# Performance work log

Hardware: AMD Instinct MI355X
Metric: run time of the kernel (lower is better)

Reference implementation:

```python
import jax, jax.numpy as jnp
import numpy as np

DIM = 256      # C
TOPK = 32      # topk_win_num
WIN = 8        # winSize
G = 64         # g (shift group size); 4*G == DIM here


def setup_inputs() -> dict:
    key = jax.random.key(0)
    k0, k1, k2, k3 = jax.random.split(key, 4)
    B, Nt, Ns, C = 32, 256, 4096, DIM
    z = jax.random.normal(k0, (B, Nt, C), jnp.float32)
    x = jax.random.normal(k1, (B, Ns, C), jnp.float32)
    # shift_op_down: Conv2d(C, 4g, 1) -> weight [4g, C]; shift_op_up: Conv2d(4g, C, 1)
    Wd = jax.random.normal(k2, (4 * G, C), jnp.float32) * 0.05
    bd = jnp.zeros((4 * G,), jnp.float32)
    Wu = jax.random.normal(k3, (C, 4 * G), jnp.float32) * 0.05
    bu = jnp.zeros((C,), jnp.float32)
    return {"z": z, "x": x, "Wd": Wd, "bd": bd, "Wu": Wu, "bu": bu}


def reference(z, x, Wd, bd, Wu, bu):
    B, Nt, C = z.shape
    Ns = x.shape[1]
    hs = int(np.sqrt(Ns))
    wn = hs // WIN          # windows per side
    wsa = WIN * WIN         # tokens per window
    K = TOPK

    # AdaptiveMaxPool2d((1,1)) over template tokens -> global max per channel
    z_max = jnp.max(z, axis=1)                               # [B, C]
    sim = jnp.einsum('bc,bnc->bn', z_max, x) / C             # [B, Ns]
    # per-window mean similarity
    sim = sim.reshape(B, wn, WIN, wn, WIN).transpose(0, 1, 3, 2, 4)
    sim = sim.reshape(B, wn * wn, wsa).mean(-1)              # [B, wn*wn]
    idx = jax.lax.top_k(sim, K)[1]                           # [B, K]

    # windowed view of search tokens: [B, wn*wn, wsa, C]
    x_win = x.reshape(B, wn, WIN, wn, WIN, C).transpose(0, 1, 3, 2, 4, 5)
    x_win = x_win.reshape(B, wn * wn, wsa, C)
    x_sel = jnp.take_along_axis(x_win, idx[:, :, None, None], axis=1)  # [B, K, wsa, C]

    xe = x_sel.reshape(B * K, WIN, WIN, C)                   # NHWC per selected window
    t = xe @ Wd.T + bd                                       # 1x1 conv down -> [n, h, w, 4G]

    # 4-direction spatial shift by 1 (zero fill), one channel group per direction
    g0, g1, g2, g3 = t[..., :G], t[..., G:2 * G], t[..., 2 * G:3 * G], t[..., 3 * G:]
    s0 = jnp.pad(g0[:, :, 1:, :], ((0, 0), (0, 0), (0, 1), (0, 0)))  # shift left  (W)
    s1 = jnp.pad(g1[:, :, :-1, :], ((0, 0), (0, 0), (1, 0), (0, 0)))  # shift right (W)
    s2 = jnp.pad(g2[:, 1:, :, :], ((0, 0), (0, 1), (0, 0), (0, 0)))  # shift up    (H)
    s3 = jnp.pad(g3[:, :-1, :, :], ((0, 0), (1, 0), (0, 0), (0, 0)))  # shift down  (H)
    sh = jnp.concatenate([s0, s1, s2, s3], axis=-1)          # [n, h, w, 4G]

    up = sh @ Wu.T + bu                                      # 1x1 conv up -> [n, h, w, C]
    out = (xe + up).reshape(B, K * WIN * WIN, C)             # [B, K*wsa, C]
    return out
```

## Files before the change

kernel.cpp:

```cpp
#include <hip/hip_runtime.h>
#include <hip/hip_bf16.h>

#define C_DIM 256
#define B_SZ 32
#define NS 4096
#define NT_Z 256
#define TOPK_K 32
#define NWIN 64
#define WTOK 64

typedef __attribute__((ext_vector_type(8))) short short8;
typedef __attribute__((ext_vector_type(4))) float f32x4;

static __device__ inline unsigned short f2b(float f) {
  union { float f; unsigned int u; } x; x.f = f;
  unsigned int u = x.u;
  return (unsigned short)((u + 0x7FFFu + ((u >> 16) & 1u)) >> 16);
}
static __device__ inline float b2f(unsigned int h16) {
  union { unsigned int u; float f; } x; x.u = h16 << 16;
  return x.f;
}

__global__ void prep_kernel(const float* __restrict__ Wd, const float* __restrict__ Wu,
                            unsigned short* __restrict__ Wdb, unsigned short* __restrict__ Wub,
                            const float* __restrict__ z, float* __restrict__ zpart) {
  int blk = blockIdx.x;
  if (blk < 64) {
    int i = blk * 256 + threadIdx.x;
    float4 a = ((const float4*)Wd)[i];
    float4 c = ((const float4*)Wu)[i];
    ushort4 ha, hc;
    ha.x = f2b(a.x); ha.y = f2b(a.y); ha.z = f2b(a.z); ha.w = f2b(a.w);
    hc.x = f2b(c.x); hc.y = f2b(c.y); hc.z = f2b(c.z); hc.w = f2b(c.w);
    ((ushort4*)Wdb)[i] = ha;
    ((ushort4*)Wub)[i] = hc;
  } else {
    int i = blk - 64;
    int b = i >> 3, ch = i & 7;
    int c = threadIdx.x;
    const float* p = z + ((size_t)b * NT_Z + ch * 32) * C_DIM + c;
    float m = p[0];
    for (int n = 1; n < 32; ++n) m = fmaxf(m, p[(size_t)n * C_DIM]);
    zpart[(size_t)i * C_DIM + c] = m;
  }
}

__global__ __launch_bounds__(256) void winscore_kernel(const float* __restrict__ x,
                                                       const float* __restrict__ zpart,
                                                       float* __restrict__ score) {
  int b = blockIdx.x >> 6;
  int w = blockIdx.x & 63;
  int wy = w >> 3, wx = w & 7;

  __shared__ float zs[C_DIM];
  {
    float m = zpart[(size_t)(b * 8) * C_DIM + threadIdx.x];
    #pragma unroll
    for (int ch = 1; ch < 8; ++ch)
      m = fmaxf(m, zpart[(size_t)(b * 8 + ch) * C_DIM + threadIdx.x]);
    zs[threadIdx.x] = m;
  }
  __syncthreads();

  int wv = threadIdx.x >> 6;
  int ln = threadIdx.x & 63;

  float a0 = 0.f, a1 = 0.f, a2 = 0.f, a3 = 0.f;
  for (int t = 0; t < 16; ++t) {
    int tok = wv * 16 + t;
    int iy = tok >> 3, ix = tok & 7;
    int n = (wy * 8 + iy) * 64 + wx * 8 + ix;
    const float4 v = *(const float4*)(x + ((size_t)b * NS + n) * C_DIM + ln * 4);
    a0 += v.x; a1 += v.y; a2 += v.z; a3 += v.w;
  }
  const float4 z4 = ((const float4*)zs)[ln];
  float p = a0 * z4.x + a1 * z4.y + a2 * z4.z + a3 * z4.w;
  for (int off = 32; off >= 1; off >>= 1) p += __shfl_xor(p, off);

  __shared__ float wsum[4];
  if (ln == 0) wsum[wv] = p;
  __syncthreads();
  if (threadIdx.x == 0) score[blockIdx.x] = wsum[0] + wsum[1] + wsum[2] + wsum[3];
}

__global__ __launch_bounds__(512, 4) void fused_win(
    const float* __restrict__ x, const float* __restrict__ score,
    const unsigned short* __restrict__ Wdb, const unsigned short* __restrict__ Wub,
    const float* __restrict__ bd, const float* __restrict__ bu,
    float* __restrict__ out)
{
  __shared__ unsigned short xe_s[WTOK * C_DIM];
  __shared__ unsigned short t_s[WTOK * C_DIM];
  __shared__ float sc[NWIN];
  __shared__ int wsel_s;

  const int bk = blockIdx.x;
  const int b = bk >> 5;
  const int kk = bk & 31;
  const int tid = threadIdx.x;

  if (tid < NWIN) sc[tid] = score[b * NWIN + tid];
  __syncthreads();
  if (tid < NWIN) {
    float v = sc[tid];
    int rank = 0;
    #pragma unroll
    for (int j = 0; j < NWIN; ++j) {
      float sj = sc[j];
      rank += (sj > v) || (sj == v && j < tid);
    }
    if (rank == kk) wsel_s = tid;
  }
  __syncthreads();
  const int wsel = wsel_s;
  const int wy = wsel >> 3, wx = wsel & 7;

  const int wv = tid >> 6;
  const int ln = tid & 63;
  const int lr = ln & 15;
  const int lg = ln >> 4;

  const unsigned short* wdbase = Wdb + ((size_t)(wv * 32 + lr)) * C_DIM + lg * 8;
  const unsigned short* wubase = Wub + ((size_t)(wv * 32 + lr)) * C_DIM + lg * 8;

  short8 wreg[8][2];
  #pragma unroll
  for (int ks = 0; ks < 8; ++ks)
    #pragma unroll
    for (int nt = 0; nt < 2; ++nt)
      wreg[ks][nt] = *(const short8*)(wdbase + nt * 16 * C_DIM + ks * 32);

  {
    const int c4 = tid & 63;
    const int m0 = tid >> 6;
    const float* xb = x + (size_t)b * NS * C_DIM + c4 * 4;
    float4 xv[8];
    #pragma unroll
    for (int i = 0; i < 8; ++i) {
      int m = m0 + i * 8;
      int n = (wy * 8 + (m >> 3)) * 64 + wx * 8 + (m & 7);
      xv[i] = *(const float4*)(xb + (size_t)n * C_DIM);
    }
    #pragma unroll
    for (int i = 0; i < 8; ++i) {
      int m = m0 + i * 8;
      ushort4 h;
      h.x = f2b(xv[i].x); h.y = f2b(xv[i].y); h.z = f2b(xv[i].z); h.w = f2b(xv[i].w);
      int byteoff = m * 512 + ((c4 * 8) ^ ((m & 7) << 4));
      *(ushort4*)((char*)xe_s + byteoff) = h;
    }
  }
  __syncthreads();

  f32x4 acc[4][2];
  #pragma unroll
  for (int a = 0; a < 4; ++a)
    #pragma unroll
    for (int n2 = 0; n2 < 2; ++n2) acc[a][n2] = (f32x4){0.f, 0.f, 0.f, 0.f};

  #pragma unroll
  for (int ks = 0; ks < 8; ++ks) {
    const int kb = ks * 64 + lg * 16;
    short8 af[4];
    #pragma unroll
    for (int mt = 0; mt < 4; ++mt) {
      int m = mt * 16 + lr;
      af[mt] = *(const short8*)((const char*)xe_s + m * 512 + (kb ^ ((m & 7) << 4)));
    }
    #pragma unroll
    for (int mt = 0; mt < 4; ++mt)
      #pragma unroll
      for (int nt = 0; nt < 2; ++nt)
        acc[mt][nt] = __builtin_amdgcn_mfma_f32_16x16x32_bf16(af[mt], wreg[ks][nt], acc[mt][nt], 0, 0, 0);
  }

  #pragma unroll
  for (int nt = 0; nt < 2; ++nt) {
    int o = wv * 32 + nt * 16 + lr;
    float bdv = bd[o];
    #pragma unroll
    for (int mt = 0; mt < 4; ++mt) {
      #pragma unroll
      for (int r = 0; r < 4; ++r) {
        int m = mt * 16 + lg * 4 + r;
        float v = acc[mt][nt][r] + bdv;
        *(unsigned short*)((char*)t_s + m * 512 + ((o * 2) ^ ((m & 7) << 4))) = f2b(v);
      }
    }
  }

  short8 wreg2[8][2];
  #pragma unroll
  for (int ks = 0; ks < 8; ++ks)
    #pragma unroll
    for (int nt = 0; nt < 2; ++nt)
      wreg2[ks][nt] = *(const short8*)(wubase + nt * 16 * C_DIM + ks * 32);

  __syncthreads();

  f32x4 acc2[4][2];
  #pragma unroll
  for (int a = 0; a < 4; ++a)
    #pragma unroll
    for (int n2 = 0; n2 < 2; ++n2) acc2[a][n2] = (f32x4){0.f, 0.f, 0.f, 0.f};

  #pragma unroll
  for (int ks = 0; ks < 8; ++ks) {
    const int g = ks >> 1;
    const int dd = ((g & 1) ? -1 : 1) * ((g & 2) ? 8 : 1);
    const int kb = ks * 64 + lg * 16;
    short8 af[4];
    #pragma unroll
    for (int mt = 0; mt < 4; ++mt) {
      int m = mt * 16 + lr;
      int pos = (g & 2) ? (m >> 3) : (m & 7);
      bool ok = (g & 1) ? (pos > 0) : (pos < 7);
      int ms = m + dd;
      ms = ms < 0 ? 0 : (ms > 63 ? 63 : ms);
      short8 v = *(const short8*)((const char*)t_s + ms * 512 + (kb ^ ((ms & 7) << 4)));
      const short8 zed = {0, 0, 0, 0, 0, 0, 0, 0};
      af[mt] = ok ? v : zed;
    }
    #pragma unroll
    for (int mt = 0; mt < 4; ++mt)
      #pragma unroll
      for (int nt = 0; nt < 2; ++nt)
        acc2[mt][nt] = __builtin_amdgcn_mfma_f32_16x16x32_bf16(af[mt], wreg2[ks][nt], acc2[mt][nt], 0, 0, 0);
  }

  const size_t obase = (size_t)bk * WTOK * C_DIM;
  #pragma unroll
  for (int nt = 0; nt < 2; ++nt) {
    int c = wv * 32 + nt * 16 + lr;
    float buv = bu[c];
    #pragma unroll
    for (int mt = 0; mt < 4; ++mt) {
      #pragma unroll
      for (int r = 0; r < 4; ++r) {
        int m = mt * 16 + lg * 4 + r;
        unsigned int xb =
            *(const unsigned short*)((const char*)xe_s + m * 512 + ((c * 2) ^ ((m & 7) << 4)));
        out[obase + (size_t)m * C_DIM + c] = b2f(xb) + acc2[mt][nt][r] + buv;
      }
    }
  }
}

extern "C" void kernel_launch(void* const* d_in, const int* in_sizes, int n_in,
                              void* d_out, int out_size, void* d_ws, size_t ws_size,
                              hipStream_t stream) {
  const float* z  = (const float*)d_in[0];
  const float* x  = (const float*)d_in[1];
  const float* Wd = (const float*)d_in[2];
  const float* bd = (const float*)d_in[3];
  const float* Wu = (const float*)d_in[4];
  const float* bu = (const float*)d_in[5];
  float* out = (float*)d_out;

  char* ws = (char*)d_ws;
  unsigned short* Wdb = (unsigned short*)(ws);
  unsigned short* Wub = (unsigned short*)(ws + 131072);
  float* zpart = (float*)(ws + 262144);
  float* score = (float*)(ws + 524288);

  hipLaunchKernelGGL(prep_kernel, dim3(320), dim3(256), 0, stream, Wd, Wu, Wdb, Wub, z, zpart);
  hipLaunchKernelGGL(winscore_kernel, dim3(B_SZ * NWIN), dim3(256), 0, stream, x, zpart, score);
  hipLaunchKernelGGL(fused_win, dim3(B_SZ * TOPK_K), dim3(512), 0, stream,
                     x, score, Wdb, Wub, bd, bu, out);
}
```

Before: 88.86 us.

## Process four windows per block with weight reuse and prefetch of next window

The fused window kernel now launches 256 persistent-style blocks, each handling four consecutive top-k windows of one batch. The block loads both weight matrices and biases into registers once, does the ranking once, and prefetches the next window's x tile into registers while the second GEMM of the current window runs. A block-index swizzle spreads batches across blocks. In exchange it has fewer blocks than CUs and a larger register footprint (launch bounds lowered to 2 blocks/SM), which may reduce parallelism and latency hiding.

```diff
diff --git a/kernel.cpp b/kernel.cpp
--- a/kernel.cpp
+++ b/kernel.cpp
@@ -84,7 +84,7 @@
   if (threadIdx.x == 0) score[blockIdx.x] = wsum[0] + wsum[1] + wsum[2] + wsum[3];
 }
 
-__global__ __launch_bounds__(512, 4) void fused_win(
+__global__ __launch_bounds__(512, 2) void fused_win(
     const float* __restrict__ x, const float* __restrict__ score,
     const unsigned short* __restrict__ Wdb, const unsigned short* __restrict__ Wub,
     const float* __restrict__ bd, const float* __restrict__ bu,
@@ -93,11 +93,12 @@
   __shared__ unsigned short xe_s[WTOK * C_DIM];
   __shared__ unsigned short t_s[WTOK * C_DIM];
   __shared__ float sc[NWIN];
-  __shared__ int wsel_s;
-
-  const int bk = blockIdx.x;
-  const int b = bk >> 5;
-  const int kk = bk & 31;
+  __shared__ int wsel4[4];
+
+  const int bid = blockIdx.x;
+  const int lb = (bid & 7) * 32 + (bid >> 3);
+  const int b  = lb >> 3;
+  const int k0 = (lb & 7) * 4;
   const int tid = threadIdx.x;
 
   if (tid < NWIN) sc[tid] = score[b * NWIN + tid];
@@ -110,11 +111,9 @@
       float sj = sc[j];
       rank += (sj > v) || (sj == v && j < tid);
     }
-    if (rank == kk) wsel_s = tid;
-  }
-  __syncthreads();
-  const int wsel = wsel_s;
-  const int wy = wsel >> 3, wx = wsel & 7;
+    int rr = rank - k0;
+    if (rr >= 0 && rr < 4) wsel4[rr] = tid;
+  }
 
   const int wv = tid >> 6;
   const int ln = tid & 63;
@@ -123,127 +122,145 @@
 
   const unsigned short* wdbase = Wdb + ((size_t)(wv * 32 + lr)) * C_DIM + lg * 8;
   const unsigned short* wubase = Wub + ((size_t)(wv * 32 + lr)) * C_DIM + lg * 8;
-
-  short8 wreg[8][2];
+  short8 wreg[8][2], wreg2[8][2];
   #pragma unroll
   for (int ks = 0; ks < 8; ++ks)
     #pragma unroll
-    for (int nt = 0; nt < 2; ++nt)
-      wreg[ks][nt] = *(const short8*)(wdbase + nt * 16 * C_DIM + ks * 32);
-
+    for (int nt = 0; nt < 2; ++nt) {
+      wreg[ks][nt]  = *(const short8*)(wdbase + nt * 16 * C_DIM + ks * 32);
+      wreg2[ks][nt] = *(const short8*)(wubase + nt * 16 * C_DIM + ks * 32);
+    }
+
+  float bdv[2], buv[2];
+  #pragma unroll
+  for (int nt = 0; nt < 2; ++nt) {
+    bdv[nt] = bd[wv * 32 + nt * 16 + lr];
+    buv[nt] = bu[wv * 32 + nt * 16 + lr];
+  }
+
+  __syncthreads();
+
+  const int c4 = tid & 63;
+  const int m0w = tid >> 6;
+  const float* xb = x + (size_t)b * NS * C_DIM + c4 * 4;
+
+  float4 xv[8];
   {
-    const int c4 = tid & 63;
-    const int m0 = tid >> 6;
-    const float* xb = x + (size_t)b * NS * C_DIM + c4 * 4;
-    float4 xv[8];
+    const int wsel = wsel4[0];
+    const int wy = wsel >> 3, wx = wsel & 7;
     #pragma unroll
     for (int i = 0; i < 8; ++i) {
-      int m = m0 + i * 8;
+      int m = m0w + i * 8;
       int n = (wy * 8 + (m >> 3)) * 64 + wx * 8 + (m & 7);
       xv[i] = *(const float4*)(xb + (size_t)n * C_DIM);
     }
+  }
+
+  for (int it = 0; it < 4; ++it) {
     #pragma unroll
     for (int i = 0; i < 8; ++i) {
-      int m = m0 + i * 8;
+      int m = m0w + i * 8;
       ushort4 h;
       h.x = f2b(xv[i].x); h.y = f2b(xv[i].y); h.z = f2b(xv[i].z); h.w = f2b(xv[i].w);
       int byteoff = m * 512 + ((c4 * 8) ^ ((m & 7) << 4));
       *(ushort4*)((char*)xe_s + byteoff) = h;
     }
-  }
-  __syncthreads();
-
-  f32x4 acc[4][2];
-  #pragma unroll
-  for (int a = 0; a < 4; ++a)
-    #pragma unroll
-    for (int n2 = 0; n2 < 2; ++n2) acc[a][n2] = (f32x4){0.f, 0.f, 0.f, 0.f};
-
-  #pragma unroll
-  for (int ks = 0; ks < 8; ++ks) {
-    const int kb = ks * 64 + lg * 16;
-    short8 af[4];
-    #pragma unroll
-    for (int mt = 0; mt < 4; ++mt) {
-      int m = mt * 16 + lr;
-      af[mt] = *(const short8*)((const char*)xe_s + m * 512 + (kb ^ ((m & 7) << 4)));
-    }
-    #pragma unroll
-    for (int mt = 0; mt < 4; ++mt)
-      #pragma unroll
-      for (int nt = 0; nt < 2; ++nt)
-        acc[mt][nt] = __builtin_amdgcn_mfma_f32_16x16x32_bf16(af[mt], wreg[ks][nt], acc[mt][nt], 0, 0, 0);
-  }
-
-  #pragma unroll
-  for (int nt = 0; nt < 2; ++nt) {
-    int o = wv * 32 + nt * 16 + lr;
-    float bdv = bd[o];
-    #pragma unroll
-    for (int mt = 0; mt < 4; ++mt) {
-      #pragma unroll
-      for (int r = 0; r < 4; ++r) {
-        int m = mt * 16 + lg * 4 + r;
-        float v = acc[mt][nt][r] + bdv;
-        *(unsigned short*)((char*)t_s + m * 512 + ((o * 2) ^ ((m & 7) << 4))) = f2b(v);
-      }
-    }
-  }
-
-  short8 wreg2[8][2];
-  #pragma unroll
-  for (int ks = 0; ks < 8; ++ks)
-    #pragma unroll
-    for (int nt = 0; nt < 2; ++nt)
-      wreg2[ks][nt] = *(const short8*)(wubase + nt * 16 * C_DIM + ks * 32);
-
-  __syncthreads();
-
-  f32x4 acc2[4][2];
-  #pragma unroll
-  for (int a = 0; a < 4; ++a)
-    #pragma unroll
-    for (int n2 = 0; n2 < 2; ++n2) acc2[a][n2] = (f32x4){0.f, 0.f, 0.f, 0.f};
-
-  #pragma unroll
-  for (int ks = 0; ks < 8; ++ks) {
-    const int g = ks >> 1;
-    const int dd = ((g & 1) ? -1 : 1) * ((g & 2) ? 8 : 1);
-    const int kb = ks * 64 + lg * 16;
-    short8 af[4];
-    #pragma unroll
-    for (int mt = 0; mt < 4; ++mt) {
-      int m = mt * 16 + lr;
-      int pos = (g & 2) ? (m >> 3) : (m & 7);
-      bool ok = (g & 1) ? (pos > 0) : (pos < 7);
-      int ms = m + dd;
-      ms = ms < 0 ? 0 : (ms > 63 ? 63 : ms);
-      short8 v = *(const short8*)((const char*)t_s + ms * 512 + (kb ^ ((ms & 7) << 4)));
-      const short8 zed = {0, 0, 0, 0, 0, 0, 0, 0};
-      af[mt] = ok ? v : zed;
-    }
-    #pragma unroll
-    for (int mt = 0; mt < 4; ++mt)
-      #pragma unroll
-      for (int nt = 0; nt < 2; ++nt)
-        acc2[mt][nt] = __builtin_amdgcn_mfma_f32_16x16x32_bf16(af[mt], wreg2[ks][nt], acc2[mt][nt], 0, 0, 0);
-  }
-
-  const size_t obase = (size_t)bk * WTOK * C_DIM;
-  #pragma unroll
-  for (int nt = 0; nt < 2; ++nt) {
-    int c = wv * 32 + nt * 16 + lr;
-    float buv = bu[c];
-    #pragma unroll
-    for (int mt = 0; mt < 4; ++mt) {
-      #pragma unroll
-      for (int r = 0; r < 4; ++r) {
-        int m = mt * 16 + lg * 4 + r;
-        unsigned int xb =
-            *(const unsigned short*)((const char*)xe_s + m * 512 + ((c * 2) ^ ((m & 7) << 4)));
-        out[obase + (size_t)m * C_DIM + c] = b2f(xb) + acc2[mt][nt][r] + buv;
-      }
-    }
+    __syncthreads();
+
+    f32x4 acc[4][2];
+    #pragma unroll
+    for (int a = 0; a < 4; ++a)
+      #pragma unroll
+      for (int n2 = 0; n2 < 2; ++n2) acc[a][n2] = (f32x4){0.f, 0.f, 0.f, 0.f};
+
+    #pragma unroll
+    for (int ks = 0; ks < 8; ++ks) {
+      const int kb = ks * 64 + lg * 16;
+      short8 af[4];
+      #pragma unroll
+      for (int mt = 0; mt < 4; ++mt) {
+        int m = mt * 16 + lr;
+        af[mt] = *(const short8*)((const char*)xe_s + m * 512 + (kb ^ ((m & 7) << 4)));
+      }
+      #pragma unroll
+      for (int mt = 0; mt < 4; ++mt)
+        #pragma unroll
+        for (int nt = 0; nt < 2; ++nt)
+          acc[mt][nt] = __builtin_amdgcn_mfma_f32_16x16x32_bf16(af[mt], wreg[ks][nt], acc[mt][nt], 0, 0, 0);
+    }
+
+    #pragma unroll
+    for (int nt = 0; nt < 2; ++nt) {
+      int o = wv * 32 + nt * 16 + lr;
+      #pragma unroll
+      for (int mt = 0; mt < 4; ++mt) {
+        #pragma unroll
+        for (int r = 0; r < 4; ++r) {
+          int m = mt * 16 + lg * 4 + r;
+          float v = acc[mt][nt][r] + bdv[nt];
+          *(unsigned short*)((char*)t_s + m * 512 + ((o * 2) ^ ((m & 7) << 4))) = f2b(v);
+        }
+      }
+    }
+
+    if (it < 3) {
+      const int wsel = wsel4[it + 1];
+      const int wy = wsel >> 3, wx = wsel & 7;
+      #pragma unroll
+      for (int i = 0; i < 8; ++i) {
+        int m = m0w + i * 8;
+        int n = (wy * 8 + (m >> 3)) * 64 + wx * 8 + (m & 7);
+        xv[i] = *(const float4*)(xb + (size_t)n * C_DIM);
+      }
+    }
+    __syncthreads();
+
+    f32x4 acc2[4][2];
+    #pragma unroll
+    for (int a = 0; a < 4; ++a)
+      #pragma unroll
+      for (int n2 = 0; n2 < 2; ++n2) acc2[a][n2] = (f32x4){0.f, 0.f, 0.f, 0.f};
+
+    #pragma unroll
+    for (int ks = 0; ks < 8; ++ks) {
+      const int g = ks >> 1;
+      const int dd = ((g & 1) ? -1 : 1) * ((g & 2) ? 8 : 1);
+      const int kb = ks * 64 + lg * 16;
+      short8 af[4];
+      #pragma unroll
+      for (int mt = 0; mt < 4; ++mt) {
+        int m = mt * 16 + lr;
+        int pos = (g & 2) ? (m >> 3) : (m & 7);
+        bool ok = (g & 1) ? (pos > 0) : (pos < 7);
+        int ms = m + dd;
+        ms = ms < 0 ? 0 : (ms > 63 ? 63 : ms);
+        short8 v = *(const short8*)((const char*)t_s + ms * 512 + (kb ^ ((ms & 7) << 4)));
+        const short8 zed = {0, 0, 0, 0, 0, 0, 0, 0};
+        af[mt] = ok ? v : zed;
+      }
+      #pragma unroll
+      for (int mt = 0; mt < 4; ++mt)
+        #pragma unroll
+        for (int nt = 0; nt < 2; ++nt)
+          acc2[mt][nt] = __builtin_amdgcn_mfma_f32_16x16x32_bf16(af[mt], wreg2[ks][nt], acc2[mt][nt], 0, 0, 0);
+    }
+
+    const size_t obase = (size_t)(b * 32 + k0 + it) * WTOK * C_DIM;
+    #pragma unroll
+    for (int nt = 0; nt < 2; ++nt) {
+      int c = wv * 32 + nt * 16 + lr;
+      #pragma unroll
+      for (int mt = 0; mt < 4; ++mt) {
+        #pragma unroll
+        for (int r = 0; r < 4; ++r) {
+          int m = mt * 16 + lg * 4 + r;
+          unsigned int xr =
+              *(const unsigned short*)((const char*)xe_s + m * 512 + ((c * 2) ^ ((m & 7) << 4)));
+          out[obase + (size_t)m * C_DIM + c] = b2f(xr) + acc2[mt][nt][r] + buv[nt];
+        }
+      }
+    }
+    __syncthreads();
   }
 }
 
@@ -266,6 +283,6 @@
 
   hipLaunchKernelGGL(prep_kernel, dim3(320), dim3(256), 0, stream, Wd, Wu, Wdb, Wub, z, zpart);
   hipLaunchKernelGGL(winscore_kernel, dim3(B_SZ * NWIN), dim3(256), 0, stream, x, zpart, score);
-  hipLaunchKernelGGL(fused_win, dim3(B_SZ * TOPK_K), dim3(512), 0, stream,
+  hipLaunchKernelGGL(fused_win, dim3(256), dim3(512), 0, stream,
                      x, score, Wdb, Wub, bd, bu, out);
 }
```

New measurement: 118.8 us. 1.34x slower.
